# Optimization experiments

Measured on AMD Instinct MI355X. Metric: run time of the kernel, lower is better.

Reference implementation:

```python
import jax, jax.numpy as jnp
import numpy as np

E, H, D = 1024, 16, 64
F = 4608          # max_ffn_size = int(1024*3*1.5)
BASE_FFN = 3072   # int(emb*3)
ADAPT = 0.5
CHUNK = 256


def rotate_half(x):
    x1 = x[..., ::2]
    x2 = x[..., 1::2]
    return jnp.stack((-x2, x1), axis=-1).reshape(x.shape[:-1] + (-1,))


def rms_norm(x, w, eps=1e-6):
    x = jnp.where(jnp.isnan(x) | jnp.isinf(x), jnp.zeros_like(x), x)
    rms = jnp.clip(jnp.sqrt(jnp.mean(x * x, axis=-1, keepdims=True) + eps), 1e-6, 1e6)
    return x / rms * w


def setup_inputs() -> dict:
    key = jax.random.key(0)
    ks = jax.random.split(key, 12)
    s = 0.02
    return {
        "x": jax.random.normal(ks[0], (2, 4096, E), dtype=jnp.float32),
        "w_qkv": jax.random.normal(ks[1], (E, 3 * E), dtype=jnp.float32) * s,
        "w_out": jax.random.normal(ks[2], (E, E), dtype=jnp.float32) * s,
        "g1": jnp.ones((E,), dtype=jnp.float32),
        "g2": jnp.ones((E,), dtype=jnp.float32),
        "w_dp1": jax.random.normal(ks[3], (E, E // 4), dtype=jnp.float32) * s,
        "w_dp2": jax.random.normal(ks[4], (E // 4, 1), dtype=jnp.float32) * s,
        "w_gate": jax.random.normal(ks[5], (E, F), dtype=jnp.float32) * s,
        "w_up": jax.random.normal(ks[6], (E, F), dtype=jnp.float32) * s,
        "w_down": jax.random.normal(ks[7], (F, E), dtype=jnp.float32) * s,
        "g_hidden": jnp.ones((F,), dtype=jnp.float32),
    }


def _linear_attention(x, w_qkv, w_out):
    B, L, _ = x.shape
    qkv = (x @ w_qkv).reshape(B, L, 3, H, D).transpose(2, 0, 3, 1, 4)  # [3,B,H,L,D]
    q, k, v = qkv[0], qkv[1], qkv[2]
    # RoPE (start_pos = 0)
    pos = jnp.arange(L, dtype=jnp.float32)
    inv_freq = 1.0 / (10000.0 ** (jnp.arange(0, D, 2, dtype=jnp.float32) / D))
    freqs = pos[:, None] * inv_freq[None, :]
    emb = jnp.concatenate([freqs, freqs], axis=-1)
    cos = jnp.cos(emb)[None, None]
    sin = jnp.sin(emb)[None, None]
    q = q * cos + rotate_half(q) * sin
    k = k * cos + rotate_half(k) * sin
    # elu + 1 feature map
    q = jax.nn.elu(q) + 1.0
    k = jax.nn.elu(k) + 1.0
    # chunk-wise cumulative recurrence (no cache path)
    NC = L // CHUNK
    def to_chunks(t):
        return jnp.moveaxis(t.reshape(B, H, NC, CHUNK, D), 2, 0)  # [NC,B,H,C,D]
    qc, kc, vc = to_chunks(q), to_chunks(k), to_chunks(v)

    def step(carry, inp):
        S, Z = carry  # S:[B,H,D,D], Z:[B,H,D]
        qi, ki, vi = inp
        kv = jnp.einsum('bhld,bhle->bhlde', ki, vi)
        kv_cum = jnp.cumsum(kv, axis=2) + S[:, :, None]
        k_cum = jnp.cumsum(ki, axis=2) + Z[:, :, None]
        num = jnp.einsum('bhld,bhlde->bhle', qi, kv_cum)
        den = jnp.einsum('bhld,bhld->bhl', qi, k_cum)
        return (kv_cum[:, :, -1], k_cum[:, :, -1]), (num, den)

    S0 = jnp.zeros((B, H, D, D), dtype=x.dtype)
    Z0 = jnp.zeros((B, H, D), dtype=x.dtype)
    _, (num, den) = jax.lax.scan(step, (S0, Z0), (qc, kc, vc))
    num = jnp.moveaxis(num, 0, 2).reshape(B, H, L, D)
    den = jnp.moveaxis(den, 0, 2).reshape(B, H, L)
    den = jnp.maximum(den, 1e-6)
    out = num / den[..., None]
    out = out.transpose(0, 2, 1, 3).reshape(B, L, H * D)
    return out @ w_out


def _adaptive_ffn(x, w_dp1, w_dp2, w_gate, w_up, w_down, g_hidden):
    x_mean = x.mean(axis=1)                                   # [B,E]
    dim_ratio = jax.nn.sigmoid(jax.nn.silu(x_mean @ w_dp1) @ w_dp2)  # [B,1]
    ratio = jnp.clip(1.0 + (dim_ratio - 0.5) * 2.0 * ADAPT, 1.0 - ADAPT, 1.0 + ADAPT)
    size = jnp.maximum(1, jnp.floor(BASE_FFN * ratio.mean())).astype(jnp.int32)
    mask = (jnp.arange(F) < size).astype(x.dtype)             # [F]
    gate = jax.nn.silu(x @ w_gate) * mask
    up = (x @ w_up) * mask
    hidden = gate * up
    hidden = jnp.where(jnp.isnan(hidden) | jnp.isinf(hidden), jnp.zeros_like(hidden), hidden)
    # RMSNorm over the first `size` features only (matches sliced torch RMSNorm)
    rms = jnp.sqrt(jnp.sum(hidden * hidden, axis=-1, keepdims=True) / size.astype(x.dtype) + 1e-6)
    rms = jnp.clip(rms, 1e-6, 1e6)
    hidden = hidden / rms * g_hidden * mask                   # padded-to-F hidden
    return hidden @ w_down


def reference(x, w_qkv, w_out, g1, g2, w_dp1, w_dp2, w_gate, w_up, w_down, g_hidden):
    # pre-norm residual block: x + attn(norm1(x)); then x + ffn(norm2(x))
    h = rms_norm(x, g1)
    x = x + _linear_attention(h, w_qkv, w_out)
    h2 = rms_norm(x, g2)
    x = x + _adaptive_ffn(h2, w_dp1, w_dp2, w_gate, w_up, w_down, g_hidden)
    return x
```

## Files before the change

kernel.cpp:

```cpp
#include <hip/hip_runtime.h>
#include <hip/hip_bf16.h>

#define Ee 1024
#define Hh 16
#define Ff 4608
#define Ll 4096
#define Bb 2
#define NCc 16
#define CHk 256

typedef short bf16x8 __attribute__((ext_vector_type(8)));
typedef float f32x4 __attribute__((ext_vector_type(4)));

#define GLD16(g, l) __builtin_amdgcn_global_load_lds( \
    (const __attribute__((address_space(1))) unsigned int*)(g), \
    (__attribute__((address_space(3))) unsigned int*)(l), 16, 0, 0)

__device__ __forceinline__ unsigned short f2bf(float f){
  unsigned int u = __builtin_bit_cast(unsigned int, f);
  u += 0x7fffu + ((u >> 16) & 1u);
  return (unsigned short)(u >> 16);
}
__device__ __forceinline__ float bf2f(unsigned short h){
  unsigned int u = ((unsigned int)h) << 16;
  return __builtin_bit_cast(float, u);
}
__device__ __forceinline__ float fixv(float v){
  return (__builtin_isnan(v) || __builtin_isinf(v)) ? 0.f : v;
}

__global__ __launch_bounds__(256) void wconv_kernel(const float* __restrict__ W,
    unsigned short* __restrict__ WT, int K, int N, const float* __restrict__ scale){
  __shared__ unsigned short T[64][72];
  int k0 = blockIdx.y*64, n0 = blockIdx.x*64;
  int t = threadIdx.x;
  int kr = t>>4, n4 = (t&15)*4;
  #pragma unroll
  for (int it=0; it<4; it++){
    int k = kr + it*16;
    float s = scale ? scale[k0+k] : 1.f;
    float4 v = *(const float4*)(W + (size_t)(k0+k)*N + n0 + n4);
    T[n4+0][k] = f2bf(v.x*s);
    T[n4+1][k] = f2bf(v.y*s);
    T[n4+2][k] = f2bf(v.z*s);
    T[n4+3][k] = f2bf(v.w*s);
  }
  __syncthreads();
  int u = t&7;
  #pragma unroll
  for (int it=0; it<2; it++){
    int n = (t>>3) + it*32;
    *(bf16x8*)(WT + (size_t)(n0+n)*K + k0 + u*8) = *(const bf16x8*)&T[n][u*8];
  }
}

__global__ __launch_bounds__(256) void rmsnorm_kernel(const float* __restrict__ x,
    const float* __restrict__ g, unsigned short* __restrict__ out){
  int row = blockIdx.x; int t = threadIdx.x;
  float4 v = ((const float4*)(x + (size_t)row*Ee))[t];
  v.x=fixv(v.x); v.y=fixv(v.y); v.z=fixv(v.z); v.w=fixv(v.w);
  float ss = v.x*v.x + v.y*v.y + v.z*v.z + v.w*v.w;
  #pragma unroll
  for (int off=32; off>0; off>>=1) ss += __shfl_down(ss, off);
  __shared__ float red[4];
  if ((t&63)==0) red[t>>6] = ss;
  __syncthreads();
  float tot = red[0]+red[1]+red[2]+red[3];
  float rms = sqrtf(tot*(1.f/Ee) + 1e-6f);
  rms = fminf(fmaxf(rms, 1e-6f), 1e6f);
  float inv = 1.f/rms;
  float4 gv = ((const float4*)g)[t];
  uint2 o;
  o.x = (unsigned)f2bf(v.x*inv*gv.x) | ((unsigned)f2bf(v.y*inv*gv.y)<<16);
  o.y = (unsigned)f2bf(v.z*inv*gv.z) | ((unsigned)f2bf(v.w*inv*gv.w)<<16);
  ((uint2*)(out + (size_t)row*Ee))[t] = o;
}

template<int MODE>
__global__ __launch_bounds__(512) void gemm_kernel(
    const unsigned short* __restrict__ A, const unsigned short* __restrict__ Bt,
    void* __restrict__ Cv, int M, int N, int K,
    const float* __restrict__ res, const float* __restrict__ rowscale,
    const float* __restrict__ klim){
  __shared__ __align__(16) unsigned short S[2][24576];
  int tid = threadIdx.x;
  int nbx = gridDim.x;
  int id = blockIdx.y * nbx + blockIdx.x;
  int chunk = (nbx * gridDim.y) >> 3;
  int wg = (id & 7) * chunk + (id >> 3);
  int m0 = (wg / nbx) * 256, n0 = (wg % nbx) * 128;
  int lane = tid & 63, wave = tid >> 6;
  int wm = (wave>>1)*64, wn = (wave&1)*64;
  int lrow = lane & 15;
  int lksw = (((lane>>4) ^ ((lrow>>1)&3)))*8;
  float klim0 = (MODE==2 && klim) ? klim[0] : 0.f;
  int kend = K;
  if (MODE==2 && klim){
    int sz = (int)klim0;
    int ke = ((sz + 63) >> 6) << 6;
    kend = ke < K ? ke : K;
  }
  int nk2 = kend >> 6;
  int segr = lane >> 2;
  int cg = (((lane&3) ^ ((lane>>3)&3))) * 8;
  const unsigned short* gp[3];
  int loff[3];
  #pragma unroll
  for (int i=0;i<3;i++){
    int g = wave*3 + i;
    if (g < 16){ gp[i] = A  + (size_t)(m0 + g*16 + segr)*K + cg;       loff[i] = g*512; }
    else       { gp[i] = Bt + (size_t)(n0 + (g-16)*16 + segr)*K + cg;  loff[i] = 8192 + (g-16)*512; }
  }
  f32x4 acc[4][4] = {};
  #pragma unroll
  for (int i=0;i<3;i++){
    GLD16(gp[i],    &S[0][loff[i]]);
    GLD16(gp[i]+32, &S[0][12288 + loff[i]]);
  }
  __syncthreads();
  int cur = 0;
  for (int t=0; t<nk2; ++t){
    if (t+1 < nk2){
      int ko = (t+1) << 6;
      #pragma unroll
      for (int i=0;i<3;i++){
        GLD16(gp[i]+ko,    &S[cur^1][loff[i]]);
        GLD16(gp[i]+ko+32, &S[cur^1][12288 + loff[i]]);
      }
    }
    #pragma unroll
    for (int kk=0; kk<2; kk++){
      int base = kk*12288;
      bf16x8 af[4], bfr[4];
      #pragma unroll
      for (int i=0;i<4;i++){
        af[i]  = *(const bf16x8*)&S[cur][base + (wm + i*16 + lrow)*32 + lksw];
        bfr[i] = *(const bf16x8*)&S[cur][base + 8192 + (wn + i*16 + lrow)*32 + lksw];
      }
      __builtin_amdgcn_s_setprio(1);
      #pragma unroll
      for (int mi=0;mi<4;mi++)
        #pragma unroll
        for (int ni=0;ni<4;ni++)
          acc[mi][ni] = __builtin_amdgcn_mfma_f32_16x16x32_bf16(af[mi], bfr[ni], acc[mi][ni], 0,0,0);
      __builtin_amdgcn_s_setprio(0);
      if (kk==0) __builtin_amdgcn_s_barrier();
    }
    __syncthreads();
    cur ^= 1;
  }
  int lg = lane >> 4;
  int rbase = m0 + wm + (lg<<2);
  int cbase = n0 + wn + lrow;
  #pragma unroll
  for (int mi=0;mi<4;mi++){
    #pragma unroll
    for (int r=0;r<4;r++){
      int row = rbase + mi*16 + r;
      float rs = 1.f;
      if (MODE==2){
        float rms = sqrtf(rowscale[row]/klim0 + 1e-6f);
        rms = fminf(fmaxf(rms, 1e-6f), 1e6f);
        rs = 1.f/rms;
      }
      #pragma unroll
      for (int ni=0;ni<4;ni++){
        int col = cbase + ni*16;
        float v = acc[mi][ni][r];
        if (MODE==0){
          ((unsigned short*)Cv)[(size_t)row*N + col] = f2bf(v);
        } else if (MODE==1){
          ((float*)Cv)[(size_t)row*N + col] = v + res[(size_t)row*N + col];
        } else {
          ((float*)Cv)[(size_t)row*N + col] = v*rs + res[(size_t)row*N + col];
        }
      }
    }
  }
}

__global__ __launch_bounds__(512) void gateup_kernel(
    const unsigned short* __restrict__ A, const unsigned short* __restrict__ Gt,
    const unsigned short* __restrict__ Ut, unsigned short* __restrict__ Hid,
    const float* __restrict__ scal, float* __restrict__ sumsq){
  __shared__ __align__(16) unsigned short S[2][32768];
  int tid = threadIdx.x;
  int nbx = gridDim.x;
  int id = blockIdx.y * nbx + blockIdx.x;
  int chunk = (nbx * gridDim.y) >> 3;
  int wg = (id & 7) * chunk + (id >> 3);
  int m0 = (wg / nbx) * 256, n0 = (wg % nbx) * 128;
  int size = (int)scal[0];
  if (n0 >= size){
    int r = tid >> 1, cb = n0 + (tid&1)*64;
    unsigned short* hp = Hid + (size_t)(m0+r)*Ff + cb;
    bf16x8 z = {};
    #pragma unroll
    for (int i=0;i<8;i++) *(bf16x8*)(hp + i*8) = z;
    return;
  }
  int lane = tid & 63, wave = tid >> 6;
  int wm = (wave>>1)*64, wn = (wave&1)*64;
  int lrow = lane & 15;
  int lksw = (((lane>>4) ^ ((lrow>>1)&3)))*8;
  int segr = lane >> 2;
  int cg = (((lane&3) ^ ((lane>>3)&3))) * 8;
  const unsigned short* gp[4];
  int loff[4];
  #pragma unroll
  for (int i=0;i<4;i++){
    int g = wave*4 + i;
    if (g < 16)      { gp[i] = A  + (size_t)(m0 + g*16 + segr)*Ee + cg;       loff[i] = g*512; }
    else if (g < 24) { gp[i] = Gt + (size_t)(n0 + (g-16)*16 + segr)*Ee + cg;  loff[i] = 8192 + (g-16)*512; }
    else             { gp[i] = Ut + (size_t)(n0 + (g-24)*16 + segr)*Ee + cg;  loff[i] = 12288 + (g-24)*512; }
  }
  f32x4 ag[4][4] = {}, au[4][4] = {};
  #pragma unroll
  for (int i=0;i<4;i++){
    GLD16(gp[i],    &S[0][loff[i]]);
    GLD16(gp[i]+32, &S[0][16384 + loff[i]]);
  }
  __syncthreads();
  int cur = 0;
  for (int t=0; t<16; ++t){
    if (t+1 < 16){
      int ko = (t+1) << 6;
      #pragma unroll
      for (int i=0;i<4;i++){
        GLD16(gp[i]+ko,    &S[cur^1][loff[i]]);
        GLD16(gp[i]+ko+32, &S[cur^1][16384 + loff[i]]);
      }
    }
    #pragma unroll
    for (int kk=0; kk<2; kk++){
      int base = kk*16384;
      bf16x8 af[4], bg4[4], bu4[4];
      #pragma unroll
      for (int i=0;i<4;i++){
        af[i]  = *(const bf16x8*)&S[cur][base + (wm + i*16 + lrow)*32 + lksw];
        bg4[i] = *(const bf16x8*)&S[cur][base + 8192  + (wn + i*16 + lrow)*32 + lksw];
        bu4[i] = *(const bf16x8*)&S[cur][base + 12288 + (wn + i*16 + lrow)*32 + lksw];
      }
      __builtin_amdgcn_s_setprio(1);
      #pragma unroll
      for (int mi=0;mi<4;mi++)
        #pragma unroll
        for (int ni=0;ni<4;ni++){
          ag[mi][ni] = __builtin_amdgcn_mfma_f32_16x16x32_bf16(af[mi], bg4[ni], ag[mi][ni], 0,0,0);
          au[mi][ni] = __builtin_amdgcn_mfma_f32_16x16x32_bf16(af[mi], bu4[ni], au[mi][ni], 0,0,0);
        }
      __builtin_amdgcn_s_setprio(0);
      if (kk==0) __builtin_amdgcn_s_barrier();
    }
    __syncthreads();
    cur ^= 1;
  }
  int lg = lane >> 4;
  int lr = lrow;
  int rbase = m0 + wm + (lg<<2);
  int cbase = n0 + wn + lr;
  #pragma unroll
  for (int mi=0;mi<4;mi++){
    #pragma unroll
    for (int r=0;r<4;r++){
      int row = rbase + mi*16 + r;
      float s4 = 0.f;
      #pragma unroll
      for (int ni=0;ni<4;ni++){
        int col = cbase + ni*16;
        float g = ag[mi][ni][r], u = au[mi][ni][r];
        float hv = (g * (1.f/(1.f+expf(-g)))) * u;
        if (col >= size) hv = 0.f;
        if (__builtin_isnan(hv) || __builtin_isinf(hv)) hv = 0.f;
        Hid[(size_t)row*Ff + col] = f2bf(hv);
        s4 += hv*hv;
      }
      s4 += __shfl_xor(s4, 1);
      s4 += __shfl_xor(s4, 2);
      s4 += __shfl_xor(s4, 4);
      s4 += __shfl_xor(s4, 8);
      if (lr == 0) atomicAdd(&sumsq[row], s4);
    }
  }
}

__global__ __launch_bounds__(256) void rope_kernel(unsigned short* __restrict__ qkv){
  size_t idx = (size_t)blockIdx.x*256 + threadIdx.x;
  int i = (int)(idx & 31);
  int h = (int)((idx>>5) & 15);
  size_t bl = idx >> 9;
  int pos = (int)(bl & (Ll-1));
  int d0 = 2*i, d1 = d0+1;
  size_t base = bl*3072 + (size_t)h*64 + d0;
  const float LOG1E4_D32 = 0.2878231366242557f;
  float e0 = (float)(d0 < 32 ? d0 : d0-32);
  float e1 = (float)(d1 < 32 ? d1 : d1-32);
  float f0 = pos * expf(-e0*LOG1E4_D32);
  float f1 = pos * expf(-e1*LOG1E4_D32);
  float s0,c0,s1,c1;
  sincosf(f0,&s0,&c0); sincosf(f1,&s1,&c1);
  unsigned int* qp = (unsigned int*)(qkv + base);
  unsigned int qv = *qp;
  float q0 = bf2f((unsigned short)(qv&0xffff)), q1 = bf2f((unsigned short)(qv>>16));
  float r0 = q0*c0 - q1*s0;
  float r1 = q1*c1 + q0*s1;
  r0 = r0>0.f ? r0+1.f : expf(r0);
  r1 = r1>0.f ? r1+1.f : expf(r1);
  *qp = (unsigned)f2bf(r0) | ((unsigned)f2bf(r1)<<16);
  unsigned int* kp = (unsigned int*)(qkv + base + 1024);
  unsigned int kv = *kp;
  float k0v = bf2f((unsigned short)(kv&0xffff)), k1v = bf2f((unsigned short)(kv>>16));
  float t0 = k0v*c0 - k1v*s0;
  float t1 = k1v*c1 + k0v*s1;
  t0 = t0>0.f ? t0+1.f : expf(t0);
  t1 = t1>0.f ? t1+1.f : expf(t1);
  *kp = (unsigned)f2bf(t0) | ((unsigned)f2bf(t1)<<16);
}

__global__ __launch_bounds__(256) void chunksum_kernel(const unsigned short* __restrict__ qkv,
    float* __restrict__ Ssum){
  __shared__ __align__(16) unsigned short Kt[64][72];
  __shared__ __align__(16) unsigned short Vt[80][72];
  int c = blockIdx.x, bh = blockIdx.y;
  int b = bh >> 4, h = bh & 15;
  int tid = threadIdx.x, lane = tid & 63, wave = tid >> 6;
  int lr = lane & 15, lg = lane >> 4;
  f32x4 acc[5] = {};
  {
    int r16 = tid >> 4, m4 = (tid & 15) * 4;
    unsigned short val = (r16 == 0) ? (unsigned short)0x3F80 : (unsigned short)0;
    #pragma unroll
    for (int u=0; u<4; u++) Vt[64 + r16][m4 + u] = val;
  }
  for (int t=0; t<4; ++t){
    __syncthreads();
    #pragma unroll
    for (int i=0; i<2; i++){
      int tau = tid + i*256;
      int m = tau & 63, dg = (tau >> 6) * 8;
      size_t g = ((size_t)(b*Ll + c*CHk + t*64 + m))*3072 + h*64 + dg;
      bf16x8 kv = *(const bf16x8*)(qkv + g + 1024);
      bf16x8 vv = *(const bf16x8*)(qkv + g + 2048);
      #pragma unroll
      for (int u=0; u<8; u++){
        Kt[dg+u][m] = (unsigned short)kv[u];
        Vt[dg+u][m] = (unsigned short)vv[u];
      }
    }
    __syncthreads();
    #pragma unroll
    for (int kk=0; kk<2; kk++){
      bf16x8 af = *(const bf16x8*)&Kt[wave*16 + lr][kk*32 + lg*8];
      #pragma unroll
      for (int ni=0; ni<5; ni++){
        bf16x8 vf = *(const bf16x8*)&Vt[ni*16 + lr][kk*32 + lg*8];
        acc[ni] = __builtin_amdgcn_mfma_f32_16x16x32_bf16(af, vf, acc[ni], 0,0,0);
      }
    }
  }
  float* S = Ssum + ((size_t)bh*NCc + c)*4160;
  int j = wave*16 + lg*4;
  #pragma unroll
  for (int ni=0; ni<4; ni++)
    #pragma unroll
    for (int r=0; r<4; r++)
      S[(size_t)(j+r)*64 + ni*16 + lr] = acc[ni][r];
  if (lr == 0){
    #pragma unroll
    for (int r=0; r<4; r++) S[4096 + j + r] = acc[4][r];
  }
}

__global__ __launch_bounds__(256) void prefix_kernel(const float* __restrict__ Ssum,
    float* __restrict__ Spre){
  int bh = blockIdx.x; int t = threadIdx.x;
  size_t base = (size_t)bh*NCc*4160;
  for (int e=t; e<4160; e+=256){
    float acc = 0.f;
    #pragma unroll
    for (int c=0;c<NCc;c++){
      Spre[base + (size_t)c*4160 + e] = acc;
      acc += Ssum[base + (size_t)c*4160 + e];
    }
  }
}

__global__ __launch_bounds__(256, 2) void attnout_kernel(const unsigned short* __restrict__ qkv,
    const float* __restrict__ Spre, unsigned short* __restrict__ attn){
  __shared__ __align__(16) unsigned short SpT[64][72];
  __shared__ __align__(16) unsigned short Ks[64][72];
  __shared__ __align__(16) unsigned short Vt[64][72];
  __shared__ __align__(16) unsigned short P[4][64][72];
  __shared__ float qZd[256];
  int c = blockIdx.x, bh = blockIdx.y;
  int b = bh >> 4, h = bh & 15;
  int tid = threadIdx.x, lane = tid & 63, wave = tid >> 6;
  int lr = lane & 15, lg = lane >> 4;
  const float* Sp = Spre + ((size_t)bh*NCc + c)*4160;

  {
    float zacc = 0.f;
    const unsigned short* qp = qkv + ((size_t)(b*Ll + c*CHk + tid))*3072 + (size_t)h*64;
    #pragma unroll
    for (int g8=0; g8<8; g8++){
      bf16x8 qv = *(const bf16x8*)(qp + g8*8);
      #pragma unroll
      for (int u=0; u<8; u++) zacc += bf2f((unsigned short)qv[u]) * Sp[4096 + g8*8 + u];
    }
    qZd[tid] = zacc;
  }
  #pragma unroll
  for (int i=0; i<2; i++){
    int tau = tid + i*256;
    int j = tau & 63, dg = (tau >> 6) * 8;
    const float* sp = Sp + j*64 + dg;
    #pragma unroll
    for (int u=0; u<8; u++) SpT[dg+u][j] = f2bf(sp[u]);
  }
  bf16x8 af[4][2];
  #pragma unroll
  for (int mi=0; mi<4; mi++){
    size_t qrow = ((size_t)(b*Ll + c*CHk + wave*64 + mi*16 + lr))*3072 + (size_t)h*64;
    #pragma unroll
    for (int kk=0; kk<2; kk++)
      af[mi][kk] = *(const bf16x8*)(qkv + qrow + kk*32 + lg*8);
  }
  __syncthreads();
  f32x4 accO[4][4] = {};
  #pragma unroll
  for (int kk=0; kk<2; kk++){
    #pragma unroll
    for (int ni=0; ni<4; ni++){
      bf16x8 bsp = *(const bf16x8*)&SpT[ni*16 + lr][kk*32 + lg*8];
      #pragma unroll
      for (int mi=0; mi<4; mi++)
        accO[mi][ni] = __builtin_amdgcn_mfma_f32_16x16x32_bf16(af[mi][kk], bsp, accO[mi][ni], 0,0,0);
    }
  }
  f32x4 den4[4] = {};
  for (int t=0; t<4; ++t){
    __syncthreads();
    #pragma unroll
    for (int i=0; i<2; i++){
      int tau = tid + i*256;
      int m = tau & 63, dg = (tau >> 6) * 8;
      size_t g = ((size_t)(b*Ll + c*CHk + t*64 + m))*3072 + h*64 + dg;
      *(bf16x8*)&Ks[m][dg] = *(const bf16x8*)(qkv + g + 1024);
      bf16x8 vv = *(const bf16x8*)(qkv + g + 2048);
      #pragma unroll
      for (int u=0; u<8; u++) Vt[dg+u][m] = (unsigned short)vv[u];
    }
    __syncthreads();
    if (wave < t) continue;
    f32x4 sacc[4][4] = {};
    #pragma unroll
    for (int kk=0; kk<2; kk++){
      #pragma unroll
      for (int ni=0; ni<4; ni++){
        bf16x8 kf = *(const bf16x8*)&Ks[ni*16 + lr][kk*32 + lg*8];
        #pragma unroll
        for (int mi=0; mi<4; mi++)
          sacc[mi][ni] = __builtin_amdgcn_mfma_f32_16x16x32_bf16(af[mi][kk], kf, sacc[mi][ni], 0,0,0);
      }
    }
    unsigned short (*Pw)[72] = P[wave];
    bool diag = (t == wave);
    #pragma unroll
    for (int mi=0; mi<4; mi++){
      #pragma unroll
      for (int r=0; r<4; r++){
        int q_l = mi*16 + lg*4 + r;
        float rs = 0.f;
        #pragma unroll
        for (int ni=0; ni<4; ni++){
          int m_l = ni*16 + lr;
          float v = sacc[mi][ni][r];
          if (diag && m_l > q_l) v = 0.f;
          rs += v;
          Pw[q_l][m_l] = f2bf(v);
        }
        rs += __shfl_xor(rs, 1);
        rs += __shfl_xor(rs, 2);
        rs += __shfl_xor(rs, 4);
        rs += __shfl_xor(rs, 8);
        den4[mi][r] += rs;
      }
    }
    #pragma unroll
    for (int kk=0; kk<2; kk++){
      bf16x8 pa[4], vf[4];
      #pragma unroll
      for (int mi=0; mi<4; mi++) pa[mi] = *(const bf16x8*)&Pw[mi*16 + lr][kk*32 + lg*8];
      #pragma unroll
      for (int ni=0; ni<4; ni++) vf[ni] = *(const bf16x8*)&Vt[ni*16 + lr][kk*32 + lg*8];
      #pragma unroll
      for (int mi=0; mi<4; mi++)
        #pragma unroll
        for (int ni=0; ni<4; ni++)
          accO[mi][ni] = __builtin_amdgcn_mfma_f32_16x16x32_bf16(pa[mi], vf[ni], accO[mi][ni], 0,0,0);
    }
  }
  #pragma unroll
  for (int mi=0; mi<4; mi++){
    #pragma unroll
    for (int r=0; r<4; r++){
      int q_l = mi*16 + lg*4 + r;
      float dtot = den4[mi][r] + qZd[wave*64 + q_l];
      float inv = 1.f / fmaxf(dtot, 1e-6f);
      size_t l = (size_t)(b*Ll + c*CHk + wave*64 + q_l);
      unsigned short* op = attn + l*Ee + h*64 + lr;
      #pragma unroll
      for (int ni=0; ni<4; ni++)
        op[ni*16] = f2bf(accO[mi][ni][r] * inv);
    }
  }
}

__global__ __launch_bounds__(256) void colmean1_kernel(const unsigned short* __restrict__ h2,
    float* __restrict__ partial){
  int e = blockIdx.x*256 + threadIdx.x;
  int ly = blockIdx.y;
  int b = blockIdx.z;
  int l0 = ly * 128;
  float s = 0.f;
  for (int l=l0; l<l0+128; l++) s += bf2f(h2[((size_t)(b*Ll + l))*Ee + e]);
  partial[((size_t)(b*32 + ly))*Ee + e] = s;
}
__global__ __launch_bounds__(256) void colmean2_kernel(const float* __restrict__ partial,
    float* __restrict__ xmean){
  int e = blockIdx.x*256 + threadIdx.x;
  int b = blockIdx.y;
  float s = 0.f;
  #pragma unroll
  for (int ly=0; ly<32; ly++) s += partial[((size_t)(b*32 + ly))*Ee + e];
  xmean[b*Ee + e] = s * (1.f/Ll);
}

__global__ __launch_bounds__(256) void dimpred_kernel(const float* __restrict__ xmean,
    const float* __restrict__ w_dp1, const float* __restrict__ w_dp2,
    float* __restrict__ scalars){
  __shared__ float red[256];
  __shared__ float ratio_s[2];
  int t = threadIdx.x;
  for (int b=0;b<2;b++){
    float s = 0.f;
    for (int k=0;k<1024;k++) s += xmean[b*Ee + k] * w_dp1[k*256 + t];
    float sil = s * (1.f/(1.f+expf(-s)));
    red[t] = sil * w_dp2[t];
    __syncthreads();
    for (int off=128; off>0; off>>=1){
      if (t<off) red[t] += red[t+off];
      __syncthreads();
    }
    if (t==0){
      float dr = 1.f/(1.f+expf(-red[0]));
      float ratio = 1.f + (dr-0.5f)*1.0f;
      ratio = fminf(fmaxf(ratio, 0.5f), 1.5f);
      ratio_s[b] = ratio;
    }
    __syncthreads();
  }
  if (t==0){
    float rm = 0.5f*(ratio_s[0]+ratio_s[1]);
    float size_f = floorf(3072.f * rm);
    if (size_f < 1.f) size_f = 1.f;
    scalars[0] = size_f;
  }
}

extern "C" void kernel_launch(void* const* d_in, const int* in_sizes, int n_in,
                              void* d_out, int out_size, void* d_ws, size_t ws_size,
                              hipStream_t stream){
  const float* x      = (const float*)d_in[0];
  const float* w_qkv  = (const float*)d_in[1];
  const float* w_out  = (const float*)d_in[2];
  const float* g1     = (const float*)d_in[3];
  const float* g2     = (const float*)d_in[4];
  const float* w_dp1  = (const float*)d_in[5];
  const float* w_dp2  = (const float*)d_in[6];
  const float* w_gate = (const float*)d_in[7];
  const float* w_up   = (const float*)d_in[8];
  const float* w_down = (const float*)d_in[9];
  const float* g_hid  = (const float*)d_in[10];
  float* out = (float*)d_out;

  char* w = (char*)d_ws;
  size_t o = 0;
  auto alloc = [&](size_t bytes)->char*{ char* p = w + o; o += (bytes + 255) & ~255ull; return p; };
  unsigned short* R1   = (unsigned short*)alloc((size_t)8192*1024*2);
  float*          x2   = (float*)alloc((size_t)8192*1024*4);
  char*           R2   = alloc((size_t)8192*4608*2);
  unsigned short* qkvT = (unsigned short*)alloc((size_t)3072*1024*2);
  unsigned short* outT = (unsigned short*)alloc((size_t)1024*1024*2);
  char*           W2   = alloc((size_t)3*4608*1024*2);
  float*       partial = (float*)alloc((size_t)64*1024*4);
  float*         xmean = (float*)alloc(2048*4);
  float*          scal = (float*)alloc(64);
  float*         sumsq = (float*)alloc(8192*4);

  unsigned short* qkv    = (unsigned short*)R2;
  unsigned short* hidden = (unsigned short*)R2;
  float* Ssum = (float*)W2;
  float* Spre = Ssum + (size_t)512*4160;
  unsigned short* gateT = (unsigned short*)W2;
  unsigned short* upT   = gateT + (size_t)4608*1024;
  unsigned short* downT = upT   + (size_t)4608*1024;

  wconv_kernel<<<dim3(3072/64, 1024/64),256,0,stream>>>(w_qkv, qkvT, 1024, 3072, nullptr);
  wconv_kernel<<<dim3(1024/64, 1024/64),256,0,stream>>>(w_out, outT, 1024, 1024, nullptr);

  rmsnorm_kernel<<<8192,256,0,stream>>>(x, g1, R1);
  gemm_kernel<0><<<dim3(3072/128, 8192/256),512,0,stream>>>(R1, qkvT, qkv,
      8192,3072,1024, nullptr,nullptr,nullptr);
  rope_kernel<<<16384,256,0,stream>>>(qkv);
  chunksum_kernel<<<dim3(NCc,Bb*Hh),256,0,stream>>>(qkv, Ssum);
  prefix_kernel<<<Bb*Hh,256,0,stream>>>(Ssum, Spre);
  attnout_kernel<<<dim3(NCc,Bb*Hh),256,0,stream>>>(qkv, Spre, R1);

  wconv_kernel<<<dim3(4608/64, 1024/64),256,0,stream>>>(w_gate, gateT, 1024, 4608, nullptr);
  wconv_kernel<<<dim3(4608/64, 1024/64),256,0,stream>>>(w_up,   upT,   1024, 4608, nullptr);
  wconv_kernel<<<dim3(1024/64, 4608/64),256,0,stream>>>(w_down, downT, 4608, 1024, g_hid);

  gemm_kernel<1><<<dim3(1024/128, 8192/256),512,0,stream>>>(R1, outT, x2,
      8192,1024,1024, x,nullptr,nullptr);
  rmsnorm_kernel<<<8192,256,0,stream>>>(x2, g2, R1);
  colmean1_kernel<<<dim3(4,32,2),256,0,stream>>>(R1, partial);
  colmean2_kernel<<<dim3(4,2),256,0,stream>>>(partial, xmean);
  dimpred_kernel<<<1,256,0,stream>>>(xmean, w_dp1, w_dp2, scal);
  hipMemsetAsync(sumsq, 0, 8192*sizeof(float), stream);
  gateup_kernel<<<dim3(4608/128, 8192/256),512,0,stream>>>(R1, gateT, upT, hidden, scal, sumsq);
  gemm_kernel<2><<<dim3(1024/128, 8192/256),512,0,stream>>>(hidden, downT, out,
      8192,1024,4608, x2, sumsq, scal);
}
```

Baseline: 489.3 us.

## Switch GEMM and gate-up kernels to 3-stage LDS pipeline with one barrier per step

Replaces the double-buffered 64-wide K pipeline in the generic GEMM and gate/up kernels with a triple-buffered 32-wide K ring that prefetches two stages ahead. Explicit vmcnt waits plus a single s_barrier per iteration replace the full __syncthreads, so global loads can stay in flight across iterations. The aim is to hide global-to-LDS latency and cut synchronisation cost. In exchange it uses less LDS per block but runs twice as many loop iterations, relies on hand-counted vmcnt values being correct, and in MODE 2 rounds the K limit to 32 instead of 64.

```diff
diff --git a/kernel.cpp b/kernel.cpp
--- a/kernel.cpp
+++ b/kernel.cpp
@@ -15,6 +15,8 @@
 #define GLD16(g, l) __builtin_amdgcn_global_load_lds( \
     (const __attribute__((address_space(1))) unsigned int*)(g), \
     (__attribute__((address_space(3))) unsigned int*)(l), 16, 0, 0)
+#define SCHED0() __builtin_amdgcn_sched_barrier(0)
+#define SBAR()   __builtin_amdgcn_s_barrier()
 
 __device__ __forceinline__ unsigned short f2bf(float f){
   unsigned int u = __builtin_bit_cast(unsigned int, f);
@@ -82,7 +84,7 @@
     void* __restrict__ Cv, int M, int N, int K,
     const float* __restrict__ res, const float* __restrict__ rowscale,
     const float* __restrict__ klim){
-  __shared__ __align__(16) unsigned short S[2][24576];
+  __shared__ __align__(16) unsigned short S[36864];
   int tid = threadIdx.x;
   int nbx = gridDim.x;
   int id = blockIdx.y * nbx + blockIdx.x;
@@ -97,10 +99,10 @@
   int kend = K;
   if (MODE==2 && klim){
     int sz = (int)klim0;
-    int ke = ((sz + 63) >> 6) << 6;
+    int ke = ((sz + 31) >> 5) << 5;
     kend = ke < K ? ke : K;
   }
-  int nk2 = kend >> 6;
+  int nk = kend >> 5;
   int segr = lane >> 2;
   int cg = (((lane&3) ^ ((lane>>3)&3))) * 8;
   const unsigned short* gp[3];
@@ -113,41 +115,44 @@
   }
   f32x4 acc[4][4] = {};
   #pragma unroll
-  for (int i=0;i<3;i++){
-    GLD16(gp[i],    &S[0][loff[i]]);
-    GLD16(gp[i]+32, &S[0][12288 + loff[i]]);
-  }
-  __syncthreads();
+  for (int i=0;i<3;i++) GLD16(gp[i], &S[loff[i]]);
+  if (nk > 1){
+    #pragma unroll
+    for (int i=0;i<3;i++) GLD16(gp[i]+32, &S[12288 + loff[i]]);
+  }
+  SCHED0();
+  if (nk > 1) asm volatile("s_waitcnt vmcnt(3)" ::: "memory");
+  else        asm volatile("s_waitcnt vmcnt(0)" ::: "memory");
+  SBAR(); SCHED0();
   int cur = 0;
-  for (int t=0; t<nk2; ++t){
-    if (t+1 < nk2){
-      int ko = (t+1) << 6;
-      #pragma unroll
-      for (int i=0;i<3;i++){
-        GLD16(gp[i]+ko,    &S[cur^1][loff[i]]);
-        GLD16(gp[i]+ko+32, &S[cur^1][12288 + loff[i]]);
-      }
-    }
-    #pragma unroll
-    for (int kk=0; kk<2; kk++){
-      int base = kk*12288;
-      bf16x8 af[4], bfr[4];
-      #pragma unroll
-      for (int i=0;i<4;i++){
-        af[i]  = *(const bf16x8*)&S[cur][base + (wm + i*16 + lrow)*32 + lksw];
-        bfr[i] = *(const bf16x8*)&S[cur][base + 8192 + (wn + i*16 + lrow)*32 + lksw];
-      }
-      __builtin_amdgcn_s_setprio(1);
-      #pragma unroll
-      for (int mi=0;mi<4;mi++)
-        #pragma unroll
-        for (int ni=0;ni<4;ni++)
-          acc[mi][ni] = __builtin_amdgcn_mfma_f32_16x16x32_bf16(af[mi], bfr[ni], acc[mi][ni], 0,0,0);
-      __builtin_amdgcn_s_setprio(0);
-      if (kk==0) __builtin_amdgcn_s_barrier();
-    }
-    __syncthreads();
-    cur ^= 1;
+  for (int t=0; t<nk; ++t){
+    if (t+2 < nk){
+      int stg = cur+2; if (stg>=3) stg-=3;
+      int ko = (t+2) << 5;
+      #pragma unroll
+      for (int i=0;i<3;i++) GLD16(gp[i]+ko, &S[stg*12288 + loff[i]]);
+    }
+    int base = cur*12288;
+    bf16x8 af[4], bfr[4];
+    #pragma unroll
+    for (int i=0;i<4;i++){
+      af[i]  = *(const bf16x8*)&S[base + (wm + i*16 + lrow)*32 + lksw];
+      bfr[i] = *(const bf16x8*)&S[base + 8192 + (wn + i*16 + lrow)*32 + lksw];
+    }
+    __builtin_amdgcn_s_setprio(1);
+    #pragma unroll
+    for (int mi=0;mi<4;mi++)
+      #pragma unroll
+      for (int ni=0;ni<4;ni++)
+        acc[mi][ni] = __builtin_amdgcn_mfma_f32_16x16x32_bf16(af[mi], bfr[ni], acc[mi][ni], 0,0,0);
+    __builtin_amdgcn_s_setprio(0);
+    if (t+1 < nk){
+      SCHED0();
+      if (t+2 < nk) asm volatile("s_waitcnt vmcnt(3)" ::: "memory");
+      else          asm volatile("s_waitcnt vmcnt(0)" ::: "memory");
+      SBAR(); SCHED0();
+    }
+    cur = (cur==2) ? 0 : cur+1;
   }
   int lg = lane >> 4;
   int rbase = m0 + wm + (lg<<2);
@@ -183,7 +188,7 @@
     const unsigned short* __restrict__ A, const unsigned short* __restrict__ Gt,
     const unsigned short* __restrict__ Ut, unsigned short* __restrict__ Hid,
     const float* __restrict__ scal, float* __restrict__ sumsq){
-  __shared__ __align__(16) unsigned short S[2][32768];
+  __shared__ __align__(16) unsigned short S[49152];
   int tid = threadIdx.x;
   int nbx = gridDim.x;
   int id = blockIdx.y * nbx + blockIdx.x;
@@ -216,44 +221,44 @@
   }
   f32x4 ag[4][4] = {}, au[4][4] = {};
   #pragma unroll
-  for (int i=0;i<4;i++){
-    GLD16(gp[i],    &S[0][loff[i]]);
-    GLD16(gp[i]+32, &S[0][16384 + loff[i]]);
-  }
-  __syncthreads();
+  for (int i=0;i<4;i++) GLD16(gp[i], &S[loff[i]]);
+  #pragma unroll
+  for (int i=0;i<4;i++) GLD16(gp[i]+32, &S[16384 + loff[i]]);
+  SCHED0();
+  asm volatile("s_waitcnt vmcnt(4)" ::: "memory");
+  SBAR(); SCHED0();
   int cur = 0;
-  for (int t=0; t<16; ++t){
-    if (t+1 < 16){
-      int ko = (t+1) << 6;
-      #pragma unroll
-      for (int i=0;i<4;i++){
-        GLD16(gp[i]+ko,    &S[cur^1][loff[i]]);
-        GLD16(gp[i]+ko+32, &S[cur^1][16384 + loff[i]]);
-      }
-    }
-    #pragma unroll
-    for (int kk=0; kk<2; kk++){
-      int base = kk*16384;
-      bf16x8 af[4], bg4[4], bu4[4];
-      #pragma unroll
-      for (int i=0;i<4;i++){
-        af[i]  = *(const bf16x8*)&S[cur][base + (wm + i*16 + lrow)*32 + lksw];
-        bg4[i] = *(const bf16x8*)&S[cur][base + 8192  + (wn + i*16 + lrow)*32 + lksw];
-        bu4[i] = *(const bf16x8*)&S[cur][base + 12288 + (wn + i*16 + lrow)*32 + lksw];
-      }
-      __builtin_amdgcn_s_setprio(1);
-      #pragma unroll
-      for (int mi=0;mi<4;mi++)
-        #pragma unroll
-        for (int ni=0;ni<4;ni++){
-          ag[mi][ni] = __builtin_amdgcn_mfma_f32_16x16x32_bf16(af[mi], bg4[ni], ag[mi][ni], 0,0,0);
-          au[mi][ni] = __builtin_amdgcn_mfma_f32_16x16x32_bf16(af[mi], bu4[ni], au[mi][ni], 0,0,0);
-        }
-      __builtin_amdgcn_s_setprio(0);
-      if (kk==0) __builtin_amdgcn_s_barrier();
-    }
-    __syncthreads();
-    cur ^= 1;
+  for (int t=0; t<32; ++t){
+    if (t+2 < 32){
+      int stg = cur+2; if (stg>=3) stg-=3;
+      int ko = (t+2) << 5;
+      #pragma unroll
+      for (int i=0;i<4;i++) GLD16(gp[i]+ko, &S[stg*16384 + loff[i]]);
+    }
+    int base = cur*16384;
+    bf16x8 af[4], bg4[4], bu4[4];
+    #pragma unroll
+    for (int i=0;i<4;i++){
+      af[i]  = *(const bf16x8*)&S[base + (wm + i*16 + lrow)*32 + lksw];
+      bg4[i] = *(const bf16x8*)&S[base + 8192  + (wn + i*16 + lrow)*32 + lksw];
+      bu4[i] = *(const bf16x8*)&S[base + 12288 + (wn + i*16 + lrow)*32 + lksw];
+    }
+    __builtin_amdgcn_s_setprio(1);
+    #pragma unroll
+    for (int mi=0;mi<4;mi++)
+      #pragma unroll
+      for (int ni=0;ni<4;ni++){
+        ag[mi][ni] = __builtin_amdgcn_mfma_f32_16x16x32_bf16(af[mi], bg4[ni], ag[mi][ni], 0,0,0);
+        au[mi][ni] = __builtin_amdgcn_mfma_f32_16x16x32_bf16(af[mi], bu4[ni], au[mi][ni], 0,0,0);
+      }
+    __builtin_amdgcn_s_setprio(0);
+    if (t+1 < 32){
+      SCHED0();
+      if (t+2 < 32) asm volatile("s_waitcnt vmcnt(4)" ::: "memory");
+      else          asm volatile("s_waitcnt vmcnt(0)" ::: "memory");
+      SBAR(); SCHED0();
+    }
+    cur = (cur==2) ? 0 : cur+1;
   }
   int lg = lane >> 4;
   int lr = lrow;
```

After: 482.6 us. No clear change (-1.4%).
